# Kernel tuning notes

Hardware: AMD Instinct MI355X
Metric: run time of the kernel (lower is better)

## Reference

```python
import jax, jax.numpy as jnp
from jax import lax
import numpy as np

S, N, E = 4, 50000, 800000
D_IN, D_NOISE, D_H, D_OUT = 96, 32, 32, 128
F_CAT = D_IN + D_NOISE + D_H  # 160, matches nn.Linear(input_dim+noise_dim+32, out)


def setup_inputs() -> dict:
    key = jax.random.key(0)
    ks = jax.random.split(key, 8)
    X = jax.random.normal(ks[0], (1, N, D_IN), dtype=jnp.float32)
    h = jax.random.normal(ks[1], (1, N, D_H), dtype=jnp.float32)
    # Bernoulli(0.5) noise, sampled in setup for determinism (original samples in forward)
    epsilon = (jax.random.uniform(ks[2], (S, N, D_NOISE)) < 0.5).astype(jnp.float32)
    W = jax.random.normal(ks[3], (F_CAT, D_OUT), dtype=jnp.float32) * 0.02
    b = jnp.zeros((D_OUT,), dtype=jnp.float32)
    gin_eps = jnp.zeros((), dtype=jnp.float32)  # init_eps=0, learn_eps=True
    src = jax.random.randint(ks[4], (E,), 0, N, dtype=jnp.int32)
    dst = jax.random.randint(ks[5], (E,), 0, N, dtype=jnp.int32)
    return {"X": X, "h": h, "epsilon": epsilon, "W": W, "b": b,
            "gin_eps": gin_eps, "src": src, "dst": dst}


def reference(X, h, epsilon, W, b, gin_eps, src, dst):
    # X: [1,N,D_IN] expanded to sample_size; h: [1,N,32] expanded; epsilon: [S,N,D_NOISE]
    s, n = epsilon.shape[0], X.shape[1]
    Xb = jnp.broadcast_to(X, (s, n, X.shape[2]))
    hb = jnp.broadcast_to(h, (s, n, h.shape[2]))
    x_all = jnp.concatenate([Xb, epsilon, hb], axis=2)  # [S,N,F_CAT]

    def per_sample(carry, x):  # x: [N,F_CAT]
        # GINConv('sum'): (1+eps)*x + sum_{j in N(i)} x_j, then Linear, then activation
        agg = (1.0 + gin_eps) * x + jax.ops.segment_sum(x[src], dst, num_segments=n)
        y = jax.nn.relu(agg @ W + b)           # [N,D_OUT]
        return carry, jnp.mean(y, axis=0)      # per-layer mean over nodes -> [D_OUT]

    _, means = lax.scan(per_sample, None, x_all)  # [S,D_OUT]
    # outputTensor[i] = tempdim12 broadcasts the [D_OUT] vector over the node axis
    out = jnp.broadcast_to(means[:, None, :], (s, n, W.shape[1]))
    return jax.nn.relu(out), epsilon
```

## Files before the change

kernel.cpp:

```cpp
#include <hip/hip_runtime.h>

#define N_NODES  50000
#define N_EDGES  800000
#define D_OUTF   128
#define F_PACK   256
#define NTILES   3125
#define GEMM_BLOCKS 512
#define NB1      196
#define PBX 6250
#define PBB 25000
#define PBZ 196
#define PBW 80
#define PB_TOT (PBX + PBB + PBZ + PBW + 1)

#define OUTB_F4  6400000
#define EPS_OFF  25600000L
#define INV_N    (1.0f / (float)N_NODES)

typedef __attribute__((ext_vector_type(8))) short bf16x8;
typedef __attribute__((ext_vector_type(4))) float f32x4;
typedef __attribute__((ext_vector_type(2))) float f32x2;

__device__ __forceinline__ unsigned short f2bf(float x) {
  unsigned int u = __float_as_uint(x);
  u += 0x7FFFu + ((u >> 16) & 1u);
  return (unsigned short)(u >> 16);
}
__device__ __forceinline__ unsigned int pack2(float a, float b) {
  return (unsigned int)f2bf(a) | ((unsigned int)f2bf(b) << 16);
}
__device__ __forceinline__ unsigned int spreadLo(unsigned int rep) {
  return (((rep & 0x08040201u) + 0x7F7F7F7Fu) >> 7) & 0x01010101u;
}
__device__ __forceinline__ unsigned int spreadHi(unsigned int rep) {
  return (((rep & 0x80402010u) + 0x7F7F7F7Fu) >> 7) & 0x01010101u;
}
__device__ __forceinline__ void f8acc(unsigned int w, float& a0, float& a1,
                                      float& a2, float& a3) {
  f32x2 p0 = __builtin_amdgcn_cvt_pk_f32_fp8(w, false);
  f32x2 p1 = __builtin_amdgcn_cvt_pk_f32_fp8(w, true);
  a0 += p0.x; a1 += p0.y; a2 += p1.x; a3 += p1.y;
}

__global__ void k_pack(const float* __restrict__ X, const float* __restrict__ h,
                       const float* __restrict__ eps, const float* __restrict__ W,
                       unsigned int* __restrict__ featF8,
                       unsigned int* __restrict__ epsb, int* __restrict__ cnt,
                       unsigned short* __restrict__ Wp,
                       float* __restrict__ outEps, float* __restrict__ sums,
                       int* __restrict__ done) {
  int blk = blockIdx.x, tid = threadIdx.x;
  if (blk < PBX) {
    int t = blk * 256 + tid;
    int node = t >> 5, f = (t & 31) << 2;
    float a0, a1, a2, a3;
    if (f < 96) {
      const float* p = X + node * 96 + f;
      a0 = p[0]; a1 = p[1]; a2 = p[2]; a3 = p[3];
    } else {
      const float* p = h + node * 32 + (f - 96);
      a0 = p[0]; a1 = p[1]; a2 = p[2]; a3 = p[3];
    }
    unsigned int d = __builtin_amdgcn_cvt_pk_fp8_f32(a0, a1, 0, false);
    d = __builtin_amdgcn_cvt_pk_fp8_f32(a2, a3, d, true);
    featF8[t] = d;
  } else if (blk < PBX + PBB) {
    long g = (long)(blk - PBX) * 256 + tid;
    float v = eps[g];
    outEps[g] = v;
    unsigned long long m = __ballot(v > 0.5f);
    int lane = tid & 63;
    if ((lane & 31) == 0) {
      long idx = g >> 5;
      int s = (int)(idx / N_NODES);
      int node = (int)(idx - (long)s * N_NODES);
      epsb[node * 4 + s] = (unsigned int)(m >> ((lane >> 5) * 32));
    }
  } else if (blk < PBX + PBB + PBZ) {
    int i = (blk - PBX - PBB) * 256 + tid;
    if (i < N_NODES) cnt[i] = 0;
  } else if (blk < PBX + PBB + PBZ + PBW) {
    int t = (blk - (PBX + PBB + PBZ)) * 256 + tid;
    int j = t & 7, col = (t >> 3) & 15, quad = (t >> 7) & 3, r = t >> 9;
    int kb5 = r % 5, i2 = r / 5;
    int wr;
    if (kb5 < 4) {
      int k = kb5 * 32 + quad * 8 + j;
      wr = (k < 96) ? k : k + 32;
    } else {
      wr = 96 + quad * 8 + j;
    }
    Wp[t] = f2bf(W[wr * D_OUTF + i2 * 16 + col]);
  } else {
    sums[tid] = 0.f;
    sums[tid + 256] = 0.f;
    if (tid < 2) done[tid] = 0;
  }
}

__global__ void k_hist(const int* __restrict__ dst, int* __restrict__ cnt) {
  int i = blockIdx.x * blockDim.x + threadIdx.x;
  if (i < N_EDGES) atomicAdd(&cnt[dst[i]], 1);
}

__global__ void k_scan1(const int* __restrict__ cnt, int* __restrict__ excl,
                        int* __restrict__ bsum, int* __restrict__ boff,
                        int* __restrict__ done) {
  __shared__ int wpart[4];
  __shared__ int sd[256];
  __shared__ int lastf;
  int tid = threadIdx.x, lane = tid & 63, wid = tid >> 6;
  int i = blockIdx.x * 256 + tid;
  int v = (i < N_NODES) ? cnt[i] : 0;
  int x = v;
#pragma unroll
  for (int d = 1; d < 64; d <<= 1) {
    int t = __shfl_up(x, d, 64);
    if (lane >= d) x += t;
  }
  if (lane == 63) wpart[wid] = x;
  __syncthreads();
  if (tid == 0) {
    int s = 0;
#pragma unroll
    for (int w = 0; w < 4; ++w) { int t = wpart[w]; wpart[w] = s; s += t; }
    __hip_atomic_store(&bsum[blockIdx.x], s, __ATOMIC_RELEASE,
                       __HIP_MEMORY_SCOPE_AGENT);
    int d = __hip_atomic_fetch_add(done, 1, __ATOMIC_ACQ_REL,
                                   __HIP_MEMORY_SCOPE_AGENT);
    lastf = (d == NB1 - 1);
  }
  __syncthreads();
  if (i < N_NODES) excl[i] = wpart[wid] + x - v;
  if (lastf) {
    int bv = (tid < NB1)
                 ? __hip_atomic_load(&bsum[tid], __ATOMIC_ACQUIRE,
                                     __HIP_MEMORY_SCOPE_AGENT)
                 : 0;
    sd[tid] = bv;
    __syncthreads();
    for (int d = 1; d < 256; d <<= 1) {
      int t = (tid >= d) ? sd[tid - d] : 0;
      __syncthreads();
      sd[tid] += t;
      __syncthreads();
    }
    if (tid < NB1) boff[tid] = sd[tid] - bv;
  }
}

__global__ void k_scatter(const int* __restrict__ src, const int* __restrict__ dst,
                          const int* __restrict__ excl, const int* __restrict__ boff,
                          int* __restrict__ cnt, int* __restrict__ csr) {
  int i = blockIdx.x * blockDim.x + threadIdx.x;
  if (i < N_EDGES) {
    int d = dst[i];
    int r = atomicAdd(&cnt[d], -1);
    csr[excl[d] + boff[d >> 8] + r - 1] = src[i];
  }
}

__global__ __launch_bounds__(256) void k_agg_ep(
    const uint2* __restrict__ feat2, const unsigned int* __restrict__ epsw,
    const float* __restrict__ geps_p, const int* __restrict__ excl,
    const int* __restrict__ boff, const int* __restrict__ csr,
    uint4* __restrict__ agg4) {
  int wave = (blockIdx.x * blockDim.x + threadIdx.x) >> 6;
  int lane = threadIdx.x & 63;
  int li = lane & 15, es = lane >> 4;
  if (wave >= N_NODES) return;
  int n = wave;
  float ge = 1.0f + geps_p[0];
  int wsel = li >> 2, bsh = (li & 3) * 8;

  int off_n = excl[n] + boff[n >> 8];
  int e1 = (n == N_NODES - 1) ? N_EDGES : excl[n + 1] + boff[(n + 1) >> 8];

  uint2 sf = feat2[n * 16 + li];
  unsigned int swd = epsw[n * 4 + wsel];

  float af0 = 0.f, af1 = 0.f, af2 = 0.f, af3 = 0.f;
  float af4 = 0.f, af5 = 0.f, af6 = 0.f, af7 = 0.f;
  unsigned int accLo = 0, accHi = 0;

  int e = off_n + es;
  for (; e + 4 < e1; e += 8) {
    int s0 = csr[e], s1 = csr[e + 4];
    uint2 f0 = feat2[s0 * 16 + li];
    uint2 f1 = feat2[s1 * 16 + li];
    unsigned int w0 = epsw[s0 * 4 + wsel];
    unsigned int w1 = epsw[s1 * 4 + wsel];
    f8acc(f0.x, af0, af1, af2, af3);  f8acc(f0.y, af4, af5, af6, af7);
    f8acc(f1.x, af0, af1, af2, af3);  f8acc(f1.y, af4, af5, af6, af7);
    unsigned int B0 = (w0 >> bsh) & 0xFFu;
    unsigned int B1 = (w1 >> bsh) & 0xFFu;
    unsigned int r0 = B0 | (B0 << 8);  r0 |= r0 << 16;
    unsigned int r1 = B1 | (B1 << 8);  r1 |= r1 << 16;
    accLo += spreadLo(r0) + spreadLo(r1);
    accHi += spreadHi(r0) + spreadHi(r1);
  }
  if (e < e1) {
    int s0 = csr[e];
    uint2 f0 = feat2[s0 * 16 + li];
    unsigned int w0 = epsw[s0 * 4 + wsel];
    f8acc(f0.x, af0, af1, af2, af3);  f8acc(f0.y, af4, af5, af6, af7);
    unsigned int B0 = (w0 >> bsh) & 0xFFu;
    unsigned int r0 = B0 | (B0 << 8);  r0 |= r0 << 16;
    accLo += spreadLo(r0);
    accHi += spreadHi(r0);
  }

#pragma unroll
  for (int d = 16; d < 64; d <<= 1) {
    af0 += __shfl_xor(af0, d, 64);  af1 += __shfl_xor(af1, d, 64);
    af2 += __shfl_xor(af2, d, 64);  af3 += __shfl_xor(af3, d, 64);
    af4 += __shfl_xor(af4, d, 64);  af5 += __shfl_xor(af5, d, 64);
    af6 += __shfl_xor(af6, d, 64);  af7 += __shfl_xor(af7, d, 64);
    accLo += __shfl_xor((int)accLo, d, 64);
    accHi += __shfl_xor((int)accHi, d, 64);
  }

  if (es == 0) {
    f32x2 s0 = __builtin_amdgcn_cvt_pk_f32_fp8(sf.x, false);
    f32x2 s1 = __builtin_amdgcn_cvt_pk_f32_fp8(sf.x, true);
    f32x2 s2 = __builtin_amdgcn_cvt_pk_f32_fp8(sf.y, false);
    f32x2 s3 = __builtin_amdgcn_cvt_pk_f32_fp8(sf.y, true);
    af0 += ge * s0.x;  af1 += ge * s0.y;
    af2 += ge * s1.x;  af3 += ge * s1.y;
    af4 += ge * s2.x;  af5 += ge * s2.y;
    af6 += ge * s3.x;  af7 += ge * s3.y;
    unsigned int Bself = (swd >> bsh) & 0xFFu;
    float ev0 = ge * (float)(Bself & 1u)        + (float)(accLo & 0xFFu);
    float ev1 = ge * (float)((Bself >> 1) & 1u) + (float)((accLo >> 8) & 0xFFu);
    float ev2 = ge * (float)((Bself >> 2) & 1u) + (float)((accLo >> 16) & 0xFFu);
    float ev3 = ge * (float)((Bself >> 3) & 1u) + (float)((accLo >> 24) & 0xFFu);
    float ev4 = ge * (float)((Bself >> 4) & 1u) + (float)(accHi & 0xFFu);
    float ev5 = ge * (float)((Bself >> 5) & 1u) + (float)((accHi >> 8) & 0xFFu);
    float ev6 = ge * (float)((Bself >> 6) & 1u) + (float)((accHi >> 16) & 0xFFu);
    float ev7 = ge * (float)((Bself >> 7) & 1u) + (float)((accHi >> 24) & 0xFFu);

    uint4 oXh, oEp;
    oXh.x = pack2(af0, af1); oXh.y = pack2(af2, af3);
    oXh.z = pack2(af4, af5); oXh.w = pack2(af6, af7);
    oEp.x = pack2(ev0, ev1); oEp.y = pack2(ev2, ev3);
    oEp.z = pack2(ev4, ev5); oEp.w = pack2(ev6, ev7);
    agg4[n * 32 + li]      = oXh;
    agg4[n * 32 + 16 + li] = oEp;
  }
}

__global__ __launch_bounds__(256) void k_gemm(const unsigned short* __restrict__ agg,
    const unsigned short* __restrict__ Wp, const float* __restrict__ b,
    float* __restrict__ sums) {
  int tid = threadIdx.x;
  int lane = tid & 63;
  int w = tid >> 6;
  int col = lane & 15;
  int quad = lane >> 4;

  const bf16x8* wp8 = (const bf16x8*)Wp;
  bf16x8 Bsh[2][4];
  bf16x8 Bep[2];
  float bias[2];
#pragma unroll
  for (int i = 0; i < 2; ++i) {
    int i2 = 2 * w + i;
    bias[i] = b[i2 * 16 + col];
#pragma unroll
    for (int kb = 0; kb < 4; ++kb)
      Bsh[i][kb] = wp8[((i2 * 5 + kb) * 4 + quad) * 16 + col];
    Bep[i] = wp8[((i2 * 5 + 4) * 4 + quad) * 16 + col];
  }

  f32x4 psum[4][2];
#pragma unroll
  for (int s = 0; s < 4; ++s)
#pragma unroll
    for (int i = 0; i < 2; ++i) psum[s][i] = (f32x4){0.f, 0.f, 0.f, 0.f};

  for (int t = blockIdx.x; t < NTILES; t += gridDim.x) {
    const unsigned short* arow = agg + (long)(t * 16 + col) * F_PACK;
    bf16x8 Ash[4];
#pragma unroll
    for (int kb = 0; kb < 4; ++kb)
      Ash[kb] = *(const bf16x8*)(arow + kb * 32 + quad * 8);
    f32x4 csh[2];
    csh[0] = (f32x4){0.f, 0.f, 0.f, 0.f};
    csh[1] = (f32x4){0.f, 0.f, 0.f, 0.f};
#pragma unroll
    for (int kb = 0; kb < 4; ++kb) {
      csh[0] = __builtin_amdgcn_mfma_f32_16x16x32_bf16(Ash[kb], Bsh[0][kb], csh[0], 0, 0, 0);
      csh[1] = __builtin_amdgcn_mfma_f32_16x16x32_bf16(Ash[kb], Bsh[1][kb], csh[1], 0, 0, 0);
    }
#pragma unroll
    for (int s = 0; s < 4; ++s) {
      bf16x8 Aep = *(const bf16x8*)(arow + 128 + s * 32 + quad * 8);
#pragma unroll
      for (int i = 0; i < 2; ++i) {
        f32x4 c = __builtin_amdgcn_mfma_f32_16x16x32_bf16(Aep, Bep[i], csh[i], 0, 0, 0);
#pragma unroll
        for (int r = 0; r < 4; ++r)
          psum[s][i][r] += fmaxf(c[r] + bias[i], 0.f);
      }
    }
  }

#pragma unroll
  for (int s = 0; s < 4; ++s)
#pragma unroll
    for (int i = 0; i < 2; ++i) {
      float v = psum[s][i][0] + psum[s][i][1] + psum[s][i][2] + psum[s][i][3];
      v += __shfl_xor(v, 16, 64);
      v += __shfl_xor(v, 32, 64);
      if (quad == 0)
        atomicAdd(&sums[s * 128 + (2 * w + i) * 16 + col], v);
    }
}

__global__ void k_out(const float* __restrict__ sums, float* __restrict__ out) {
  int i = blockIdx.x * 256 + threadIdx.x;
  int o4 = i & 31;
  unsigned int sn = (unsigned int)i >> 5;
  unsigned int s = sn / (unsigned int)N_NODES;
  float4 sv = ((const float4*)sums)[s * 32 + o4];
  float4 ov;
  ov.x = fmaxf(sv.x * INV_N, 0.f);
  ov.y = fmaxf(sv.y * INV_N, 0.f);
  ov.z = fmaxf(sv.z * INV_N, 0.f);
  ov.w = fmaxf(sv.w * INV_N, 0.f);
  ((float4*)out)[i] = ov;
}

extern "C" void kernel_launch(void* const* d_in, const int* in_sizes, int n_in,
                              void* d_out, int out_size, void* d_ws, size_t ws_size,
                              hipStream_t stream) {
  const float* X    = (const float*)d_in[0];
  const float* h    = (const float*)d_in[1];
  const float* eps  = (const float*)d_in[2];
  const float* W    = (const float*)d_in[3];
  const float* b    = (const float*)d_in[4];
  const float* geps = (const float*)d_in[5];
  const int*   src  = (const int*)d_in[6];
  const int*   dst  = (const int*)d_in[7];
  float* out = (float*)d_out;

  char* w = (char*)d_ws;
  unsigned int*  featF8 = (unsigned int*)w;  w += (size_t)N_NODES * 32 * 4;
  unsigned int*  epsb   = (unsigned int*)w;  w += (size_t)N_NODES * 4 * 4;
  unsigned int*  agg_u  = (unsigned int*)w;  w += (size_t)N_NODES * 128 * 4;
  int*   excl     = (int*)w;   w += (size_t)(N_NODES + 16) * 4;
  int*   cnt      = (int*)w;   w += (size_t)N_NODES * 4;
  int*   csr      = (int*)w;   w += (size_t)N_EDGES * 4;
  int*   bsum     = (int*)w;   w += 256 * 4;
  int*   boff     = (int*)w;   w += 256 * 4;
  unsigned short* Wp = (unsigned short*)w; w += (size_t)20480 * 2;
  float* sums     = (float*)w; w += 512 * 4;
  int*   done     = (int*)w;   w += 64;

  int eb = (N_EDGES + 255) / 256;
  k_pack<<<PB_TOT, 256, 0, stream>>>(X, h, eps, W, featF8, epsb, cnt, Wp,
                                     out + EPS_OFF, sums, done);
  k_hist<<<eb, 256, 0, stream>>>(dst, cnt);
  k_scan1<<<NB1, 256, 0, stream>>>(cnt, excl, bsum, boff, &done[0]);
  k_scatter<<<eb, 256, 0, stream>>>(src, dst, excl, boff, cnt, csr);

  k_agg_ep<<<(N_NODES * 64) / 256, 256, 0, stream>>>((const uint2*)featF8, epsb,
                                                     geps, excl, boff, csr,
                                                     (uint4*)agg_u);

  k_gemm<<<GEMM_BLOCKS, 256, 0, stream>>>((const unsigned short*)agg_u, Wp, b,
                                          sums);

  k_out<<<OUTB_F4 / 256, 256, 0, stream>>>(sums, out);
}
```

Before: 331.7 us.

## Fuse histogram into pack kernel and double-buffer GEMM tiles through LDS

The edge-count histogram moves into the pack kernel as an extra block range, and the count array is zeroed with a memset instead, which removes one kernel launch. The GEMM now runs 512 threads per block, one output column group per wave. Each 16-row tile is staged into a padded, double-buffered LDS array, with the next tile prefetched into registers while the current one is computed. This aims to cut redundant global loads of the same A rows across waves and to hide load latency, at the cost of LDS use and a barrier per tile.

```diff
diff --git a/kernel.cpp b/kernel.cpp
--- a/kernel.cpp
+++ b/kernel.cpp
@@ -5,13 +5,13 @@
 #define D_OUTF   128
 #define F_PACK   256
 #define NTILES   3125
-#define GEMM_BLOCKS 512
+#define GEMM_BLOCKS 256
 #define NB1      196
 #define PBX 6250
 #define PBB 25000
-#define PBZ 196
+#define PBH 3125
 #define PBW 80
-#define PB_TOT (PBX + PBB + PBZ + PBW + 1)
+#define PB_TOT (PBX + PBB + PBH + PBW + 1)
 
 #define OUTB_F4  6400000
 #define EPS_OFF  25600000L
@@ -44,6 +44,7 @@
 
 __global__ void k_pack(const float* __restrict__ X, const float* __restrict__ h,
                        const float* __restrict__ eps, const float* __restrict__ W,
+                       const int* __restrict__ dst,
                        unsigned int* __restrict__ featF8,
                        unsigned int* __restrict__ epsb, int* __restrict__ cnt,
                        unsigned short* __restrict__ Wp,
@@ -76,11 +77,11 @@
       int node = (int)(idx - (long)s * N_NODES);
       epsb[node * 4 + s] = (unsigned int)(m >> ((lane >> 5) * 32));
     }
-  } else if (blk < PBX + PBB + PBZ) {
+  } else if (blk < PBX + PBB + PBH) {
     int i = (blk - PBX - PBB) * 256 + tid;
-    if (i < N_NODES) cnt[i] = 0;
-  } else if (blk < PBX + PBB + PBZ + PBW) {
-    int t = (blk - (PBX + PBB + PBZ)) * 256 + tid;
+    atomicAdd(&cnt[dst[i]], 1);
+  } else if (blk < PBX + PBB + PBH + PBW) {
+    int t = (blk - (PBX + PBB + PBH)) * 256 + tid;
     int j = t & 7, col = (t >> 3) & 15, quad = (t >> 7) & 3, r = t >> 9;
     int kb5 = r % 5, i2 = r / 5;
     int wr;
@@ -96,11 +97,6 @@
     sums[tid + 256] = 0.f;
     if (tid < 2) done[tid] = 0;
   }
-}
-
-__global__ void k_hist(const int* __restrict__ dst, int* __restrict__ cnt) {
-  int i = blockIdx.x * blockDim.x + threadIdx.x;
-  if (i < N_EDGES) atomicAdd(&cnt[dst[i]], 1);
 }
 
 __global__ void k_scan1(const int* __restrict__ cnt, int* __restrict__ excl,
@@ -249,9 +245,10 @@
   }
 }
 
-__global__ __launch_bounds__(256) void k_gemm(const unsigned short* __restrict__ agg,
+__global__ __launch_bounds__(512) void k_gemm(const uint4* __restrict__ agg4,
     const unsigned short* __restrict__ Wp, const float* __restrict__ b,
     float* __restrict__ sums) {
+  __shared__ uint4 lds[2][544];
   int tid = threadIdx.x;
   int lane = tid & 63;
   int w = tid >> 6;
@@ -259,62 +256,68 @@
   int quad = lane >> 4;
 
   const bf16x8* wp8 = (const bf16x8*)Wp;
-  bf16x8 Bsh[2][4];
-  bf16x8 Bep[2];
-  float bias[2];
-#pragma unroll
-  for (int i = 0; i < 2; ++i) {
-    int i2 = 2 * w + i;
-    bias[i] = b[i2 * 16 + col];
+  bf16x8 Bsh[4], Bep;
+  float bias = b[w * 16 + col];
+#pragma unroll
+  for (int kb = 0; kb < 4; ++kb)
+    Bsh[kb] = wp8[((w * 5 + kb) * 4 + quad) * 16 + col];
+  Bep = wp8[((w * 5 + 4) * 4 + quad) * 16 + col];
+
+  int p1 = tid, row1 = p1 / 33, c1 = p1 - row1 * 33;
+  int p2 = 512 + tid, row2 = p2 / 33, c2 = p2 - row2 * 33;
+  bool v1 = (c1 < 32);
+  bool v2 = (tid < 16) && (c2 < 32);
+
+  f32x4 psum[4];
+#pragma unroll
+  for (int s = 0; s < 4; ++s) psum[s] = (f32x4){0.f, 0.f, 0.f, 0.f};
+
+  {
+    int t0 = blockIdx.x;
+    if (v1) lds[0][p1] = agg4[t0 * 512 + row1 * 32 + c1];
+    if (v2) lds[0][p2] = agg4[t0 * 512 + row2 * 32 + c2];
+  }
+  int cur = 0;
+  for (int t = blockIdx.x; t < NTILES; t += GEMM_BLOCKS) {
+    int t2 = t + GEMM_BLOCKS;
+    if (t2 >= NTILES) t2 = t;
+    uint4 r1, r2;
+    if (v1) r1 = agg4[t2 * 512 + row1 * 32 + c1];
+    if (v2) r2 = agg4[t2 * 512 + row2 * 32 + c2];
+
+    __syncthreads();
+
+    const uint4* base = &lds[cur][col * 33];
+    bf16x8 Ash[4];
 #pragma unroll
     for (int kb = 0; kb < 4; ++kb)
-      Bsh[i][kb] = wp8[((i2 * 5 + kb) * 4 + quad) * 16 + col];
-    Bep[i] = wp8[((i2 * 5 + 4) * 4 + quad) * 16 + col];
-  }
-
-  f32x4 psum[4][2];
-#pragma unroll
-  for (int s = 0; s < 4; ++s)
-#pragma unroll
-    for (int i = 0; i < 2; ++i) psum[s][i] = (f32x4){0.f, 0.f, 0.f, 0.f};
-
-  for (int t = blockIdx.x; t < NTILES; t += gridDim.x) {
-    const unsigned short* arow = agg + (long)(t * 16 + col) * F_PACK;
-    bf16x8 Ash[4];
+      Ash[kb] = *(const bf16x8*)(base + kb * 4 + quad);
+    f32x4 csh = (f32x4){0.f, 0.f, 0.f, 0.f};
 #pragma unroll
     for (int kb = 0; kb < 4; ++kb)
-      Ash[kb] = *(const bf16x8*)(arow + kb * 32 + quad * 8);
-    f32x4 csh[2];
-    csh[0] = (f32x4){0.f, 0.f, 0.f, 0.f};
-    csh[1] = (f32x4){0.f, 0.f, 0.f, 0.f};
-#pragma unroll
-    for (int kb = 0; kb < 4; ++kb) {
-      csh[0] = __builtin_amdgcn_mfma_f32_16x16x32_bf16(Ash[kb], Bsh[0][kb], csh[0], 0, 0, 0);
-      csh[1] = __builtin_amdgcn_mfma_f32_16x16x32_bf16(Ash[kb], Bsh[1][kb], csh[1], 0, 0, 0);
-    }
+      csh = __builtin_amdgcn_mfma_f32_16x16x32_bf16(Ash[kb], Bsh[kb], csh, 0, 0, 0);
 #pragma unroll
     for (int s = 0; s < 4; ++s) {
-      bf16x8 Aep = *(const bf16x8*)(arow + 128 + s * 32 + quad * 8);
-#pragma unroll
-      for (int i = 0; i < 2; ++i) {
-        f32x4 c = __builtin_amdgcn_mfma_f32_16x16x32_bf16(Aep, Bep[i], csh[i], 0, 0, 0);
-#pragma unroll
-        for (int r = 0; r < 4; ++r)
-          psum[s][i][r] += fmaxf(c[r] + bias[i], 0.f);
-      }
-    }
-  }
-
-#pragma unroll
-  for (int s = 0; s < 4; ++s)
-#pragma unroll
-    for (int i = 0; i < 2; ++i) {
-      float v = psum[s][i][0] + psum[s][i][1] + psum[s][i][2] + psum[s][i][3];
-      v += __shfl_xor(v, 16, 64);
-      v += __shfl_xor(v, 32, 64);
-      if (quad == 0)
-        atomicAdd(&sums[s * 128 + (2 * w + i) * 16 + col], v);
-    }
+      bf16x8 Aep = *(const bf16x8*)(base + 16 + s * 4 + quad);
+      f32x4 c = __builtin_amdgcn_mfma_f32_16x16x32_bf16(Aep, Bep, csh, 0, 0, 0);
+#pragma unroll
+      for (int r = 0; r < 4; ++r)
+        psum[s][r] += fmaxf(c[r] + bias, 0.f);
+    }
+
+    if (v1) lds[cur ^ 1][p1] = r1;
+    if (v2) lds[cur ^ 1][p2] = r2;
+    cur ^= 1;
+  }
+
+#pragma unroll
+  for (int s = 0; s < 4; ++s) {
+    float v = psum[s][0] + psum[s][1] + psum[s][2] + psum[s][3];
+    v += __shfl_xor(v, 16, 64);
+    v += __shfl_xor(v, 32, 64);
+    if (quad == 0)
+      atomicAdd(&sums[s * 128 + w * 16 + col], v);
+  }
 }
 
 __global__ void k_out(const float* __restrict__ sums, float* __restrict__ out) {
@@ -358,9 +361,9 @@
   int*   done     = (int*)w;   w += 64;
 
   int eb = (N_EDGES + 255) / 256;
-  k_pack<<<PB_TOT, 256, 0, stream>>>(X, h, eps, W, featF8, epsb, cnt, Wp,
+  hipMemsetAsync(cnt, 0, (size_t)N_NODES * 4, stream);
+  k_pack<<<PB_TOT, 256, 0, stream>>>(X, h, eps, W, dst, featF8, epsb, cnt, Wp,
                                      out + EPS_OFF, sums, done);
-  k_hist<<<eb, 256, 0, stream>>>(dst, cnt);
   k_scan1<<<NB1, 256, 0, stream>>>(cnt, excl, bsum, boff, &done[0]);
   k_scatter<<<eb, 256, 0, stream>>>(src, dst, excl, boff, cnt, csr);
 
@@ -368,8 +371,7 @@
                                                      geps, excl, boff, csr,
                                                      (uint4*)agg_u);
 
-  k_gemm<<<GEMM_BLOCKS, 256, 0, stream>>>((const unsigned short*)agg_u, Wp, b,
-                                          sums);
+  k_gemm<<<GEMM_BLOCKS, 512, 0, stream>>>((const uint4*)agg_u, Wp, b, sums);
 
   k_out<<<OUTB_F4 / 256, 256, 0, stream>>>(sums, out);
 }
```

Result: faster. 319.4 us, median of 2 (-3.7%).
